# Kernel tuning notes

Measured on AMD Instinct MI355X. Metric: run time of the kernel, lower is better.

The kernel has to match this reference:

```python
import jax, jax.numpy as jnp
import numpy as np

N_NODES = 10000
NEG_SLOPE_ATT = 0.5   # GATConv negative_slope
NEG_SLOPE_ACT = 0.01  # F.leaky_relu default used as self.act


def setup_inputs() -> dict:
    key = jax.random.key(0)
    k1, k2, k3, k4, k5 = jax.random.split(key, 5)
    in_dim, out_dim = 512, 128
    x = jax.random.normal(k1, (N_NODES, in_dim), dtype=jnp.float32)
    edge_index = jax.random.randint(k2, (2, 320000), 0, N_NODES, dtype=jnp.int64)
    # glorot-ish scaled params
    W = jax.random.normal(k3, (in_dim, out_dim), dtype=jnp.float32) * (1.0 / np.sqrt(in_dim))
    att_src = jax.random.normal(k4, (out_dim,), dtype=jnp.float32) * (1.0 / np.sqrt(out_dim))
    att_dst = jax.random.normal(k5, (out_dim,), dtype=jnp.float32) * (1.0 / np.sqrt(out_dim))
    bias = jnp.zeros((out_dim,), dtype=jnp.float32)
    return {"x": x, "edge_index": edge_index, "W": W,
            "att_src": att_src, "att_dst": att_dst, "bias": bias}


def _leaky(v, slope):
    return jnp.where(v >= 0, v, slope * v)


def reference(x, edge_index, W, att_src, att_dst, bias):
    N = x.shape[0]
    loop = jnp.arange(N, dtype=edge_index.dtype)
    src = jnp.concatenate([edge_index[0], loop])  # message source j
    dst = jnp.concatenate([edge_index[1], loop])  # message target i

    h = x @ W                      # [N, out_dim]
    a_src = h @ att_src            # [N]
    a_dst = h @ att_dst            # [N]

    e = _leaky(a_src[src] + a_dst[dst], NEG_SLOPE_ATT)   # [E+N]
    # segment softmax over incoming edges of each dst node
    m = jax.ops.segment_max(e, dst, num_segments=N)
    ex = jnp.exp(e - m[dst])
    denom = jax.ops.segment_sum(ex, dst, num_segments=N)
    alpha = ex / denom[dst]

    out = jax.ops.segment_sum(h[src] * alpha[:, None], dst, num_segments=N) + bias
    embed_x = _leaky(out, NEG_SLOPE_ACT)                 # self.act = F.leaky_relu
    recon = jax.nn.sigmoid(embed_x @ embed_x.T)          # [N, N]
    return recon, embed_x
```

## Files before the change

### kernel.cpp

```cpp
#include <hip/hip_runtime.h>
#include <stdint.h>


typedef __attribute__((ext_vector_type(8))) short short8v;
typedef __attribute__((ext_vector_type(4))) float f32x4;

#define IN_DIM 512
#define OUT_DIM 128
#define NEG_ATT 0.5f
#define NEG_ACT 0.01f

__device__ __forceinline__ float leakyf(float v, float s) { return v >= 0.f ? v : s * v; }

__device__ __forceinline__ uint16_t f2bf(float v) {
  uint32_t u = __float_as_uint(v);
  u += 0x7FFFu + ((u >> 16) & 1u);
  return (uint16_t)(u >> 16);
}
__device__ __forceinline__ float bf2f(uint16_t b) { return __uint_as_float(((uint32_t)b) << 16); }

__global__ __launch_bounds__(256) void k_h_gemm(const float* __restrict__ x,
                                                const float* __restrict__ W,
                                                const float* __restrict__ att_s_g,
                                                const float* __restrict__ att_d_g,
                                                const int* __restrict__ e_dst,
                                                int* __restrict__ cnt, int E,
                                                uint16_t* __restrict__ h16,
                                                float* __restrict__ a_src,
                                                float* __restrict__ a_dst, int N) {
  int tid = threadIdx.x;
  int tx = tid & 31, ty = tid >> 5;
  int row0 = blockIdx.x * 16 + ty * 2;
  int rc[2];
  #pragma unroll
  for (int r = 0; r < 2; ++r) rc[r] = (row0 + r < N) ? (row0 + r) : (N - 1);

  f32x4 acc[2];
  #pragma unroll
  for (int r = 0; r < 2; ++r) acc[r] = (f32x4){0.f, 0.f, 0.f, 0.f};

  for (int k = 0; k < IN_DIM; k += 4) {
    f32x4 wreg[4];
    #pragma unroll
    for (int kk = 0; kk < 4; ++kk)
      wreg[kk] = *(const f32x4*)&W[(size_t)(k + kk) * OUT_DIM + tx * 4];
    #pragma unroll
    for (int r = 0; r < 2; ++r) {
      f32x4 xv = *(const f32x4*)&x[(size_t)rc[r] * IN_DIM + k];
      #pragma unroll
      for (int kk = 0; kk < 4; ++kk) {
        acc[r][0] = fmaf(xv[kk], wreg[kk][0], acc[r][0]);
        acc[r][1] = fmaf(xv[kk], wreg[kk][1], acc[r][1]);
        acc[r][2] = fmaf(xv[kk], wreg[kk][2], acc[r][2]);
        acc[r][3] = fmaf(xv[kk], wreg[kk][3], acc[r][3]);
      }
    }
  }

  float atts[4], attd[4];
  #pragma unroll
  for (int j = 0; j < 4; ++j) { atts[j] = att_s_g[tx * 4 + j]; attd[j] = att_d_g[tx * 4 + j]; }
  #pragma unroll
  for (int r = 0; r < 2; ++r) {
    int row = row0 + r;
    float ps = 0.f, pd = 0.f;
    #pragma unroll
    for (int j = 0; j < 4; ++j) { ps = fmaf(acc[r][j], atts[j], ps); pd = fmaf(acc[r][j], attd[j], pd); }
    #pragma unroll
    for (int off = 16; off; off >>= 1) {
      ps += __shfl_xor(ps, off);
      pd += __shfl_xor(pd, off);
    }
    if (row < N) {
      uint32_t lo = (uint32_t)f2bf(acc[r][0]) | ((uint32_t)f2bf(acc[r][1]) << 16);
      uint32_t hi = (uint32_t)f2bf(acc[r][2]) | ((uint32_t)f2bf(acc[r][3]) << 16);
      uint2 pk; pk.x = lo; pk.y = hi;
      *(uint2*)&h16[(size_t)row * OUT_DIM + tx * 4] = pk;
      if (tx == 0) { a_src[row] = ps; a_dst[row] = pd; }
    }
  }

  int e0 = blockIdx.x * 512 + tid;
  if (e0 < E) atomicAdd(&cnt[e_dst[e0]], 1);
  int e1 = e0 + 256;
  if (e1 < E) atomicAdd(&cnt[e_dst[e1]], 1);
}

__global__ __launch_bounds__(1024) void k_scan(const int* __restrict__ cnt,
                                               int* __restrict__ row_start,
                                               int* __restrict__ cursor, int N) {
  __shared__ int sd[1024];
  int t = threadIdx.x;
  const int CH = (N + 1023) >> 10;
  int base = t * CH;
  int s = 0;
  for (int k = 0; k < CH; ++k) { int i = base + k; if (i < N) s += cnt[i]; }
  sd[t] = s;
  __syncthreads();
  for (int off = 1; off < 1024; off <<= 1) {
    int v = (t >= off) ? sd[t - off] : 0;
    __syncthreads();
    sd[t] += v;
    __syncthreads();
  }
  int run = (t == 0) ? 0 : sd[t - 1];
  for (int k = 0; k < CH; ++k) {
    int i = base + k;
    if (i < N) { row_start[i] = run; cursor[i] = run; run += cnt[i]; }
  }
  if (t == 1023) row_start[N] = sd[1023];
}
__global__ void k_fill(const int* __restrict__ src, const int* __restrict__ dst,
                       int* __restrict__ cursor, int* __restrict__ csr, int E) {
  int e = blockIdx.x * blockDim.x + threadIdx.x;
  if (e < E) {
    int d = dst[e];
    int pos = atomicAdd(&cursor[d], 1);
    csr[pos] = src[e];
  }
}

__global__ __launch_bounds__(256) void k_aggregate(
    const uint16_t* __restrict__ h16, const float* __restrict__ a_src,
    const float* __restrict__ a_dst, const int* __restrict__ row_start,
    const int* __restrict__ csr, const float* __restrict__ bias,
    float* __restrict__ embed_out, uint16_t* __restrict__ ebf, int N, int NPAD) {
  int wid = (int)((blockIdx.x * blockDim.x + threadIdx.x) >> 6);
  int lane = threadIdx.x & 63;
  if (wid >= N) {
    if (wid < NPAD) {
      ebf[(size_t)wid * OUT_DIM + lane] = 0;
      ebf[(size_t)wid * OUT_DIM + 64 + lane] = 0;
    }
    return;
  }
  int i = wid;
  int s0 = row_start[i], s1 = row_start[i + 1];
  float adst = a_dst[i];
  float eself = leakyf(a_src[i] + adst, NEG_ATT);
  float m = eself;
  for (int k = s0 + lane; k < s1; k += 64) {
    float e = leakyf(a_src[csr[k]] + adst, NEG_ATT);
    m = fmaxf(m, e);
  }
  #pragma unroll
  for (int off = 32; off; off >>= 1) m = fmaxf(m, __shfl_xor(m, off));
  float dsum = 0.f;
  for (int k = s0 + lane; k < s1; k += 64) {
    float e = leakyf(a_src[csr[k]] + adst, NEG_ATT);
    dsum += __expf(e - m);
  }
  #pragma unroll
  for (int off = 32; off; off >>= 1) dsum += __shfl_xor(dsum, off);
  dsum += __expf(eself - m);
  float inv = 1.0f / dsum;
  float wself = __expf(eself - m) * inv;
  float acc0 = bf2f(h16[(size_t)i * OUT_DIM + lane]) * wself;
  float acc1 = bf2f(h16[(size_t)i * OUT_DIM + 64 + lane]) * wself;
  #pragma unroll 4
  for (int k = s0; k < s1; ++k) {
    int s = csr[k];
    float w = __expf(leakyf(a_src[s] + adst, NEG_ATT) - m) * inv;
    acc0 = fmaf(bf2f(h16[(size_t)s * OUT_DIM + lane]), w, acc0);
    acc1 = fmaf(bf2f(h16[(size_t)s * OUT_DIM + 64 + lane]), w, acc1);
  }
  float o0 = leakyf(acc0 + bias[lane], NEG_ACT);
  float o1 = leakyf(acc1 + bias[64 + lane], NEG_ACT);
  embed_out[(size_t)i * OUT_DIM + lane] = o0;
  embed_out[(size_t)i * OUT_DIM + 64 + lane] = o1;
  ebf[(size_t)i * OUT_DIM + lane] = f2bf(o0);
  ebf[(size_t)i * OUT_DIM + 64 + lane] = f2bf(o1);
}

__global__ __launch_bounds__(512, 6) void k_recon(const uint16_t* __restrict__ ebf,
                                                  float* __restrict__ out,
                                                  int N, int nb) {
  __shared__ __align__(16) unsigned char smem[49152];
  uint16_t* sA = (uint16_t*)smem;
  uint16_t* sB = (uint16_t*)(smem + 32768);
  float* sO = (float*)smem;

  int tid = threadIdx.x;
  int wid = tid >> 6, lane = tid & 63;
  int wr = wid >> 2, wc = wid & 3;
  int r16 = lane & 15, kg = lane >> 4;

  int nwg = nb * nb;
  int q = nwg >> 3, r8 = nwg & 7;
  int orig = blockIdx.x;
  int xcd = orig & 7, sub = orig >> 3;
  int swz = (xcd < r8 ? xcd * (q + 1) : r8 * (q + 1) + (xcd - r8) * q) + sub;
  int by = swz / nb, bx = swz - by * nb;
  int rowBlk = by * 128, colBlk = bx * 128;

  #pragma unroll
  for (int p = 0; p < 4; ++p) {
    int i2 = p * 512 + tid;
    int row = i2 >> 4, slot = i2 & 15;
    f32x4 va = *(const f32x4*)&ebf[(size_t)(rowBlk + row) * OUT_DIM + slot * 8];
    int ss = slot ^ (row & 7);
    *(f32x4*)&sA[row * OUT_DIM + ss * 8] = va;
  }
  #pragma unroll
  for (int p = 0; p < 2; ++p) {
    int i2 = p * 512 + tid;
    int row = i2 >> 3, slot = i2 & 7;
    f32x4 vb = *(const f32x4*)&ebf[(size_t)(colBlk + row) * OUT_DIM + slot * 8];
    int ss = slot ^ (row & 7);
    *(f32x4*)&sB[row * 64 + ss * 8] = vb;
  }
  __syncthreads();

  int rowWl = wr * 64, colWl = wc * 32;
  f32x4 acc[4][2];
  #pragma unroll
  for (int a = 0; a < 4; ++a)
    #pragma unroll
    for (int b = 0; b < 2; ++b) acc[a][b] = (f32x4){0.f, 0.f, 0.f, 0.f};

  #pragma unroll
  for (int half = 0; half < 2; ++half) {
    #pragma unroll
    for (int kch = 0; kch < 2; ++kch) {
      int s16 = (half * 2 + kch) * 4 + kg;
      int khalf = kch * 4 + kg;
      short8v bfr[2];
      #pragma unroll
      for (int tj = 0; tj < 2; ++tj) {
        int rw = colWl + tj * 16 + r16;
        int ss = khalf ^ (rw & 7);
        bfr[tj] = *(const short8v*)&sB[rw * 64 + ss * 8];
      }
      #pragma unroll
      for (int ti = 0; ti < 4; ++ti) {
        int rw = rowWl + ti * 16 + r16;
        int ss = s16 ^ (rw & 7);
        short8v af = *(const short8v*)&sA[rw * OUT_DIM + ss * 8];
        #pragma unroll
        for (int tj = 0; tj < 2; ++tj)
          acc[ti][tj] = __builtin_amdgcn_mfma_f32_16x16x32_bf16(af, bfr[tj], acc[ti][tj], 0, 0, 0);
      }
    }
    if (half == 0) {
      __syncthreads();
      #pragma unroll
      for (int p = 0; p < 2; ++p) {
        int i2 = p * 512 + tid;
        int row = i2 >> 3, slot = i2 & 7;
        f32x4 vb = *(const f32x4*)&ebf[(size_t)(colBlk + row) * OUT_DIM + 64 + slot * 8];
        int ss = slot ^ (row & 7);
        *(f32x4*)&sB[row * 64 + ss * 8] = vb;
      }
      __syncthreads();
    }
  }
  __syncthreads();

  bool colFull = (colBlk + 128 <= N);
  #pragma unroll
  for (int s = 0; s < 2; ++s) {
    if (wr == s) {
      #pragma unroll
      for (int ti = 0; ti < 4; ++ti)
        #pragma unroll
        for (int tj = 0; tj < 2; ++tj) {
          int col = wc * 32 + tj * 16 + r16;
          int slot = col >> 2, within = col & 3;
          int sslot = slot ^ (kg << 1);
          #pragma unroll
          for (int qq = 0; qq < 4; ++qq)
            sO[(ti * 16 + kg * 4 + qq) * 128 + sslot * 4 + within] = acc[ti][tj][qq];
        }
    }
    __syncthreads();
    int srow0 = rowBlk + s * 64;
    #pragma unroll
    for (int p = 0; p < 4; ++p) {
      int i2 = p * 512 + tid;
      int row = i2 >> 5, c = i2 & 31;
      int sslot = c ^ (((row >> 2) & 3) << 1);
      f32x4 v = *(const f32x4*)&sO[row * 128 + sslot * 4];
      #pragma unroll
      for (int j = 0; j < 4; ++j) v[j] = 1.0f / (1.0f + __expf(-v[j]));
      int rr = srow0 + row;
      if (rr < N) {
        int col = colBlk + c * 4;
        if (colFull) {
          __builtin_nontemporal_store(v, (f32x4*)&out[(size_t)rr * N + col]);
        } else {
          #pragma unroll
          for (int j = 0; j < 4; ++j)
            if (col + j < N) __builtin_nontemporal_store(v[j], &out[(size_t)rr * N + col + j]);
        }
      }
    }
    if (s == 0) __syncthreads();
  }
}

extern "C" void kernel_launch(void* const* d_in, const int* in_sizes, int n_in,
                              void* d_out, int out_size, void* d_ws, size_t ws_size,
                              hipStream_t stream) {
  const float* x = (const float*)d_in[0];
  const int* ei = (const int*)d_in[1];
  const float* W = (const float*)d_in[2];
  const float* att_s = (const float*)d_in[3];
  const float* att_d = (const float*)d_in[4];
  const float* bias = (const float*)d_in[5];

  const int N = in_sizes[0] / IN_DIM;
  const int E = in_sizes[1] / 2;
  const int NB = (N + 127) / 128;
  const int NPAD = NB * 128;

  float* out = (float*)d_out;
  float* embed_out = out + (size_t)N * N;

  uint16_t* h16 = (uint16_t*)d_ws;
  float* a_src = (float*)(h16 + (size_t)N * OUT_DIM);
  float* a_dst = a_src + N;
  int* cnt = (int*)(a_dst + N);
  int* row_start = cnt + N;
  int* cursor = row_start + (N + 4);
  int* csr = cursor + N;
  uint16_t* ebf = (uint16_t*)(csr + E);

  const int* e_src = ei;
  const int* e_dst = ei + E;

  hipMemsetAsync(cnt, 0, (size_t)N * sizeof(int), stream);
  k_h_gemm<<<dim3((N + 15) / 16), 256, 0, stream>>>(x, W, att_s, att_d,
                                                    e_dst, cnt, E, h16, a_src, a_dst, N);
  k_scan<<<dim3(1), 1024, 0, stream>>>(cnt, row_start, cursor, N);
  k_fill<<<dim3((E + 255) / 256), 256, 0, stream>>>(e_src, e_dst, cursor, csr, E);
  k_aggregate<<<dim3((NPAD * 64 + 255) / 256), 256, 0, stream>>>(
      h16, a_src, a_dst, row_start, csr, bias, embed_out, ebf, N, NPAD);
  k_recon<<<dim3(NB * NB), 512, 0, stream>>>(ebf, out, N, NB);
}
```

Before: 225.1 us.

## Widen recon tile to 128x256 and apply sigmoid before LDS staging

The reconstruction GEMM tile doubles from 128x128 to 128x256 columns, so each warp now computes 64x64 with 16 accumulators. This halves the number of workgroups and A-tile reloads, and amortizes the A loads over more MFMAs. The sigmoid moves into the accumulator-to-LDS write, which now uses a new XOR swizzle on a 256-wide output buffer. In exchange, LDS grows to 64KB and register pressure rises, so occupancy drops (launch bound min blocks 6 to 4). Padding of the embedding buffer changes to a multiple of 256.

```diff
diff --git a/kernel.cpp b/kernel.cpp
--- a/kernel.cpp
+++ b/kernel.cpp
@@ -172,10 +172,10 @@
   ebf[(size_t)i * OUT_DIM + 64 + lane] = f2bf(o1);
 }
 
-__global__ __launch_bounds__(512, 6) void k_recon(const uint16_t* __restrict__ ebf,
+__global__ __launch_bounds__(512, 4) void k_recon(const uint16_t* __restrict__ ebf,
                                                   float* __restrict__ out,
-                                                  int N, int nb) {
-  __shared__ __align__(16) unsigned char smem[49152];
+                                                  int N, int nbR, int nbC) {
+  __shared__ __align__(16) unsigned char smem[65536];
   uint16_t* sA = (uint16_t*)smem;
   uint16_t* sB = (uint16_t*)(smem + 32768);
   float* sO = (float*)smem;
@@ -185,13 +185,13 @@
   int wr = wid >> 2, wc = wid & 3;
   int r16 = lane & 15, kg = lane >> 4;
 
-  int nwg = nb * nb;
+  int nwg = nbR * nbC;
   int q = nwg >> 3, r8 = nwg & 7;
   int orig = blockIdx.x;
   int xcd = orig & 7, sub = orig >> 3;
   int swz = (xcd < r8 ? xcd * (q + 1) : r8 * (q + 1) + (xcd - r8) * q) + sub;
-  int by = swz / nb, bx = swz - by * nb;
-  int rowBlk = by * 128, colBlk = bx * 128;
+  int by = swz / nbC, bx = swz - by * nbC;
+  int rowBlk = by * 128, colBlk = bx * 256;
 
   #pragma unroll
   for (int p = 0; p < 4; ++p) {
@@ -202,7 +202,7 @@
     *(f32x4*)&sA[row * OUT_DIM + ss * 8] = va;
   }
   #pragma unroll
-  for (int p = 0; p < 2; ++p) {
+  for (int p = 0; p < 4; ++p) {
     int i2 = p * 512 + tid;
     int row = i2 >> 3, slot = i2 & 7;
     f32x4 vb = *(const f32x4*)&ebf[(size_t)(colBlk + row) * OUT_DIM + slot * 8];
@@ -211,12 +211,12 @@
   }
   __syncthreads();
 
-  int rowWl = wr * 64, colWl = wc * 32;
-  f32x4 acc[4][2];
+  int rowWl = wr * 64, colWl = wc * 64;
+  f32x4 acc[4][4];
   #pragma unroll
   for (int a = 0; a < 4; ++a)
     #pragma unroll
-    for (int b = 0; b < 2; ++b) acc[a][b] = (f32x4){0.f, 0.f, 0.f, 0.f};
+    for (int b = 0; b < 4; ++b) acc[a][b] = (f32x4){0.f, 0.f, 0.f, 0.f};
 
   #pragma unroll
   for (int half = 0; half < 2; ++half) {
@@ -224,9 +224,9 @@
     for (int kch = 0; kch < 2; ++kch) {
       int s16 = (half * 2 + kch) * 4 + kg;
       int khalf = kch * 4 + kg;
-      short8v bfr[2];
-      #pragma unroll
-      for (int tj = 0; tj < 2; ++tj) {
+      short8v bfr[4];
+      #pragma unroll
+      for (int tj = 0; tj < 4; ++tj) {
         int rw = colWl + tj * 16 + r16;
         int ss = khalf ^ (rw & 7);
         bfr[tj] = *(const short8v*)&sB[rw * 64 + ss * 8];
@@ -237,14 +237,14 @@
         int ss = s16 ^ (rw & 7);
         short8v af = *(const short8v*)&sA[rw * OUT_DIM + ss * 8];
         #pragma unroll
-        for (int tj = 0; tj < 2; ++tj)
+        for (int tj = 0; tj < 4; ++tj)
           acc[ti][tj] = __builtin_amdgcn_mfma_f32_16x16x32_bf16(af, bfr[tj], acc[ti][tj], 0, 0, 0);
       }
     }
     if (half == 0) {
       __syncthreads();
       #pragma unroll
-      for (int p = 0; p < 2; ++p) {
+      for (int p = 0; p < 4; ++p) {
         int i2 = p * 512 + tid;
         int row = i2 >> 3, slot = i2 & 7;
         f32x4 vb = *(const f32x4*)&ebf[(size_t)(colBlk + row) * OUT_DIM + 64 + slot * 8];
@@ -256,35 +256,33 @@
   }
   __syncthreads();
 
-  bool colFull = (colBlk + 128 <= N);
+  bool colFull = (colBlk + 256 <= N);
   #pragma unroll
   for (int s = 0; s < 2; ++s) {
     if (wr == s) {
       #pragma unroll
       for (int ti = 0; ti < 4; ++ti)
         #pragma unroll
-        for (int tj = 0; tj < 2; ++tj) {
-          int col = wc * 32 + tj * 16 + r16;
-          int slot = col >> 2, within = col & 3;
-          int sslot = slot ^ (kg << 1);
+        for (int tj = 0; tj < 4; ++tj) {
+          int col = wc * 64 + tj * 16 + r16;
           #pragma unroll
-          for (int qq = 0; qq < 4; ++qq)
-            sO[(ti * 16 + kg * 4 + qq) * 128 + sslot * 4 + within] = acc[ti][tj][qq];
+          for (int qq = 0; qq < 4; ++qq) {
+            int row = ti * 16 + kg * 4 + qq;
+            float sg = 1.0f / (1.0f + __expf(-acc[ti][tj][qq]));
+            sO[row * 256 + (col ^ ((row & 4) << 2))] = sg;
+          }
         }
     }
     __syncthreads();
     int srow0 = rowBlk + s * 64;
     #pragma unroll
-    for (int p = 0; p < 4; ++p) {
+    for (int p = 0; p < 8; ++p) {
       int i2 = p * 512 + tid;
-      int row = i2 >> 5, c = i2 & 31;
-      int sslot = c ^ (((row >> 2) & 3) << 1);
-      f32x4 v = *(const f32x4*)&sO[row * 128 + sslot * 4];
-      #pragma unroll
-      for (int j = 0; j < 4; ++j) v[j] = 1.0f / (1.0f + __expf(-v[j]));
+      int row = i2 >> 6, c4 = i2 & 63;
+      f32x4 v = *(const f32x4*)&sO[row * 256 + ((c4 * 4) ^ ((row & 4) << 2))];
       int rr = srow0 + row;
       if (rr < N) {
-        int col = colBlk + c * 4;
+        int col = colBlk + c4 * 4;
         if (colFull) {
           __builtin_nontemporal_store(v, (f32x4*)&out[(size_t)rr * N + col]);
         } else {
@@ -310,8 +308,9 @@
 
   const int N = in_sizes[0] / IN_DIM;
   const int E = in_sizes[1] / 2;
-  const int NB = (N + 127) / 128;
-  const int NPAD = NB * 128;
+  const int NBR = (N + 127) / 128;
+  const int NBC = (N + 255) / 256;
+  const int NPAD = NBC * 256;
 
   float* out = (float*)d_out;
   float* embed_out = out + (size_t)N * N;
@@ -335,5 +334,5 @@
   k_fill<<<dim3((E + 255) / 256), 256, 0, stream>>>(e_src, e_dst, cursor, csr, E);
   k_aggregate<<<dim3((NPAD * 64 + 255) / 256), 256, 0, stream>>>(
       h16, a_src, a_dst, row_start, csr, bias, embed_out, ebf, N, NPAD);
-  k_recon<<<dim3(NB * NB), 512, 0, stream>>>(ebf, out, N, NB);
-}
+  k_recon<<<dim3(NBR * NBC), 512, 0, stream>>>(ebf, out, N, NBR, NBC);
+}
```

Result: slower. 230.8 us (+2.5%).
